# Performance work log

Hardware: AMD Instinct MI355X
Metric: run time of the kernel (lower is better)

The kernel has to match this reference:

```python
import jax, jax.numpy as jnp
import numpy as np

T, H, E, K = 16384, 2880, 128, 4

def setup_inputs() -> dict:
    key = jax.random.key(0)
    k1, k2, k3 = jax.random.split(key, 3)
    return {
        "hidden_states": jax.random.normal(k1, (T, H), dtype=jnp.float32),
        "weight": jax.random.normal(k2, (E, H), dtype=jnp.float32) * 0.02,
        "bias": jax.random.normal(k3, (E,), dtype=jnp.float32) * 0.02,
    }

def reference(hidden_states, weight, bias):
    x = hidden_states.reshape(-1, weight.shape[1])            # [T, H]
    logits = jnp.einsum('th,eh->te', x, weight) + bias        # [T, E]
    top_val, top_idx = jax.lax.top_k(logits, K)               # sorted desc, [T, K]
    top_val = jax.nn.softmax(top_val, axis=-1)
    rows = jnp.arange(logits.shape[0])[:, None]
    scores = jnp.zeros_like(logits).at[rows, top_idx].set(top_val)
    return scores, top_idx
```

## Files before the change

kernel.cpp:

```cpp
#include <hip/hip_runtime.h>
#include <math.h>


#define T_TOK 16384
#define HDIM  2880
#define EEXP  128
#define KTOP  4

#define TM   32
#define NT   256
#define KC   64
#define NCH  (HDIM / KC)
#define XBUF 8192
#define TAU  2.5e-4f

typedef __attribute__((ext_vector_type(8))) short bf16x8;
typedef __attribute__((ext_vector_type(4))) float f32x4;

#define MFMA(a, b, c) __builtin_amdgcn_mfma_f32_16x16x32_bf16((a), (b), (c), 0, 0, 0)

__global__ __launch_bounds__(256) void w_split(
    const float* __restrict__ w, char* __restrict__ wp)
{
    const int gid  = blockIdx.x * 256 + threadIdx.x;
    const int lane = gid & 63;
    const int q    = gid >> 6;
    const int ks   = q & 1;
    const int q2   = q >> 1;
    const int c    = q2 % NCH;
    const int F    = q2 / NCH;
    const int e    = F * 16 + (lane & 15);
    const int k0   = c * 64 + ks * 32 + (lane >> 4) * 8;

    const float* src = w + (size_t)e * HDIM + k0;
    float4 v0 = *(const float4*)(src);
    float4 v1 = *(const float4*)(src + 4);
    float vv[8] = {v0.x, v0.y, v0.z, v0.w, v1.x, v1.y, v1.z, v1.w};
    union { unsigned short s[8]; uint4 u; } H, L;
#pragma unroll
    for (int j = 0; j < 8; ++j) {
        unsigned u = __float_as_uint(vv[j]);
        H.s[j] = (unsigned short)(u >> 16);
        float rr = vv[j] - __uint_as_float(u & 0xffff0000u);
        L.s[j] = (unsigned short)(__float_as_uint(rr) >> 16);
    }
    const int tile = ((F * NCH + c) * 2 + ks) * 2;
    *(uint4*)(wp + (size_t)tile * 1024 + lane * 16)       = H.u;
    *(uint4*)(wp + (size_t)(tile + 1) * 1024 + lane * 16) = L.u;
}

static __device__ __forceinline__ void split_write256(char* base, int off, float4 v) {
    union { float4 v4; unsigned u[4]; } uv; uv.v4 = v;
    unsigned h01 = __builtin_amdgcn_perm(uv.u[1], uv.u[0], 0x07060302u);
    unsigned h23 = __builtin_amdgcn_perm(uv.u[3], uv.u[2], 0x07060302u);
    float r0 = v.x - __uint_as_float(uv.u[0] & 0xffff0000u);
    float r1 = v.y - __uint_as_float(uv.u[1] & 0xffff0000u);
    float r2 = v.z - __uint_as_float(uv.u[2] & 0xffff0000u);
    float r3 = v.w - __uint_as_float(uv.u[3] & 0xffff0000u);
    unsigned l01 = __builtin_amdgcn_perm(__float_as_uint(r1), __float_as_uint(r0), 0x07060302u);
    unsigned l23 = __builtin_amdgcn_perm(__float_as_uint(r3), __float_as_uint(r2), 0x07060302u);
    uint2 hw; hw.x = h01; hw.y = h23;
    uint2 lw; lw.x = l01; lw.y = l23;
    *(uint2*)(base + off)       = hw;
    *(uint2*)(base + off + 128) = lw;
}

__global__ __launch_bounds__(NT, 2) void router_fused(
    const float* __restrict__ x, const char* __restrict__ wp,
    const float* __restrict__ w, const float* __restrict__ bias,
    float* __restrict__ out)
{
    __shared__ char smem[20480];
    const int tid  = threadIdx.x;
    const int tok0 = blockIdx.x * TM;
    const int lane = tid & 63;
    const int wv   = tid >> 6;
    const int r    = lane & 15;
    const int g    = lane >> 4;

    char* xb0 = smem;
    char* xb1 = smem + XBUF;

    int xoff[2];
    const float* xptr[2];
#pragma unroll
    for (int i = 0; i < 2; ++i) {
        int f = tid + i * NT;
        int row = f >> 4, c4 = f & 15;
        xoff[i] = row * 256 + ((((c4 >> 1) ^ (row & 7)) << 4) | ((c4 & 1) << 3));
        xptr[i] = x + (size_t)(tok0 + row) * HDIM + c4 * 4;
    }

    int aoff[2][2];
#pragma unroll
    for (int tf = 0; tf < 2; ++tf) {
        int row = tf * 16 + r;
#pragma unroll
        for (int ks = 0; ks < 2; ++ks)
            aoff[tf][ks] = row * 256 + (((ks * 4 + g) ^ (row & 7)) << 4);
    }

    f32x4 a00 = {0.f, 0.f, 0.f, 0.f}, a01 = a00, a10 = a00, a11 = a00;

#define LOADX(pf, cc) do {                                            \
        pf[0] = *(const float4*)(xptr[0] + (cc) * KC);                \
        pf[1] = *(const float4*)(xptr[1] + (cc) * KC); } while (0)

#define WRITEX(pf, bb) do {                                           \
        split_write256((bb), xoff[0], pf[0]);                         \
        split_write256((bb), xoff[1], pf[1]); } while (0)

#define LOADW(W, cc) do {                                             \
        _Pragma("unroll")                                             \
        for (int F2 = 0; F2 < 2; ++F2)                                \
        _Pragma("unroll")                                             \
        for (int ks_ = 0; ks_ < 2; ++ks_)                             \
        _Pragma("unroll")                                             \
        for (int p_ = 0; p_ < 2; ++p_)                                \
            W[F2*4 + ks_*2 + p_] = *(const bf16x8*)(wp +              \
                (size_t)((((wv*2 + F2) * NCH + (cc)) * 2 + ks_) * 2 + p_) * 1024 \
                + lane * 16); } while (0)

#define MFMA_CHUNK(cb, W) do {                                        \
        _Pragma("unroll")                                             \
        for (int ks_ = 0; ks_ < 2; ++ks_) {                           \
            bf16x8 ah0 = *(const bf16x8*)((cb) + aoff[0][ks_]);       \
            bf16x8 al0 = *(const bf16x8*)((cb) + aoff[0][ks_] + 128); \
            bf16x8 ah1 = *(const bf16x8*)((cb) + aoff[1][ks_]);       \
            bf16x8 al1 = *(const bf16x8*)((cb) + aoff[1][ks_] + 128); \
            bf16x8 bh0 = W[ks_*2],     bl0 = W[ks_*2 + 1];            \
            bf16x8 bh1 = W[4 + ks_*2], bl1 = W[4 + ks_*2 + 1];        \
            a00 = MFMA(ah0, bh0, a00); a01 = MFMA(ah0, bh1, a01);     \
            a10 = MFMA(ah1, bh0, a10); a11 = MFMA(ah1, bh1, a11);     \
            a00 = MFMA(ah0, bl0, a00); a01 = MFMA(ah0, bl1, a01);     \
            a10 = MFMA(ah1, bl0, a10); a11 = MFMA(ah1, bl1, a11);     \
            a00 = MFMA(al0, bh0, a00); a01 = MFMA(al0, bh1, a01);     \
            a10 = MFMA(al1, bh0, a10); a11 = MFMA(al1, bh1, a11);     \
        } } while (0)

    float4 pf[2];
    bf16x8 wA[8], wB[8];

    LOADX(pf, 0);
    LOADW(wA, 0);
    WRITEX(pf, xb0);
    __syncthreads();

    for (int c = 0; c < NCH - 1; c += 2) {
        LOADX(pf, c + 1); LOADW(wB, c + 1);
        MFMA_CHUNK(xb0, wA);
        WRITEX(pf, xb1);
        __syncthreads();
        if (c + 2 < NCH) { LOADX(pf, c + 2); LOADW(wA, c + 2); }
        MFMA_CHUNK(xb1, wB);
        if (c + 2 < NCH) WRITEX(pf, xb0);
        __syncthreads();
    }
    MFMA_CHUNK(xb0, wA);
    __syncthreads();

    float* logitsL = (float*)smem;
    const float bv0 = bias[wv * 32 + r];
    const float bv1 = bias[wv * 32 + 16 + r];
#pragma unroll
    for (int q = 0; q < 4; ++q) {
        int m0 = g * 4 + q, m1 = m0 + 16;
        int e0 = wv * 32 + r, e1 = e0 + 16;
        logitsL[m0 * 130 + e0] = a00[q] + bv0;
        logitsL[m0 * 130 + e1] = a01[q] + bv1;
        logitsL[m1 * 130 + e0] = a10[q] + bv0;
        logitsL[m1 * 130 + e1] = a11[q] + bv1;
    }
    float*  cvf = (float*) (smem + 16640);
    int*    cie = (int*)   (smem + 17664);
    int*    flg = (int*)   (smem + 18688);
    double* svd = (double*)(smem + 18816);
    int*    sid = (int*)   (smem + 19840);
    double* cvd = (double*)(smem + 20352);
    __syncthreads();

    {
        const int t = tid >> 3, s = tid & 7;
        float v[8]; int id[8];
#pragma unroll
        for (int k = 0; k < 8; ++k) { v[k] = -3.4e38f; id[k] = 0x7fffffff; }
        for (int jj = 0; jj < 16; ++jj) {
            float lv = logitsL[t * 130 + s * 16 + jj];
            int   e  = s * 16 + jj;
            bool gt[8];
#pragma unroll
            for (int k = 0; k < 8; ++k)
                gt[k] = (lv > v[k]) || (lv == v[k] && e < id[k]);
#pragma unroll
            for (int k = 7; k >= 1; --k)
                if (gt[k - 1]) { v[k] = v[k - 1]; id[k] = id[k - 1]; }
#pragma unroll
            for (int k = 0; k < 8; ++k) {
                bool put = gt[k] && (k == 0 || !gt[k - 1]);
                if (put) { v[k] = lv; id[k] = e; }
            }
        }
#pragma unroll
        for (int rd = 0; rd < 8; ++rd) {
            float hv = v[0]; int hi = id[0];
#pragma unroll
            for (int off = 1; off < 8; off <<= 1) {
                float ov = __shfl_xor(hv, off);
                int   oi = __shfl_xor(hi, off);
                if (ov > hv || (ov == hv && oi < hi)) { hv = ov; hi = oi; }
            }
            if (s == 0) { cvf[t * 8 + rd] = hv; cie[t * 8 + rd] = hi; }
            bool mine = (v[0] == hv) && (id[0] == hi);
            if (mine) {
#pragma unroll
                for (int k = 0; k < 7; ++k) { v[k] = v[k + 1]; id[k] = id[k + 1]; }
                v[7] = -3.4e38f; id[7] = 0x7fffffff;
            }
        }
    }
    __syncthreads();

    if (tid < TM) {
        float gmin = 3.4e38f;
#pragma unroll
        for (int k = 0; k < 4; ++k)
            gmin = fminf(gmin, cvf[tid * 8 + k] - cvf[tid * 8 + k + 1]);
        flg[tid] = (gmin < TAU);
    }
    if (tid < 128) {
        int t2 = tid >> 2, k = tid & 3;
        svd[t2 * 4 + k] = (double)cvf[t2 * 8 + k];
        sid[t2 * 4 + k] = cie[t2 * 8 + k];
    }
    __syncthreads();

    for (int ts = 0; ts < TM; ++ts) {
        if (!flg[ts]) continue;
#pragma unroll
        for (int h2 = 0; h2 < 2; ++h2) {
            const int cand = wv * 2 + h2;
            const int ce = cie[ts * 8 + cand];
            const float4* xr = (const float4*)(x + (size_t)(tok0 + ts) * HDIM);
            const float4* wr = (const float4*)(w + (size_t)ce * HDIM);
            double q0 = 0.0, q1 = 0.0, q2 = 0.0, q3 = 0.0;
            for (int i2 = 0; i2 < 12; ++i2) {
                int fi = lane + i2 * 64;
                if (fi < HDIM / 4) {
                    float4 xv = xr[fi];
                    float4 wv4 = wr[fi];
                    q0 = fma((double)xv.x, (double)wv4.x, q0);
                    q1 = fma((double)xv.y, (double)wv4.y, q1);
                    q2 = fma((double)xv.z, (double)wv4.z, q2);
                    q3 = fma((double)xv.w, (double)wv4.w, q3);
                }
            }
            double accd = (q0 + q2) + (q1 + q3);
#pragma unroll
            for (int off = 32; off > 0; off >>= 1)
                accd += __shfl_xor(accd, off);
            if (lane == 0) cvd[cand] = accd + (double)bias[ce];
        }
        __syncthreads();
        if (tid < 8) {
            double mv = cvd[tid]; int mi2 = cie[ts * 8 + tid];
            int rk = 0;
#pragma unroll
            for (int j2 = 0; j2 < 8; ++j2) {
                double oj = cvd[j2];
                rk += (oj > mv) || (oj == mv && cie[ts * 8 + j2] < mi2);
            }
            if (rk < 4) { svd[ts * 4 + rk] = mv; sid[ts * 4 + rk] = mi2; }
        }
        __syncthreads();
    }

    float* srow = (float*)smem;
    float4 z4 = make_float4(0.f, 0.f, 0.f, 0.f);
#pragma unroll
    for (int i = 0; i < 4; ++i)
        ((float4*)srow)[tid + i * NT] = z4;
    __syncthreads();

    if (tid < TM) {
        double m  = svd[tid * 4];
        double e0 = exp(svd[tid * 4 + 0] - m), e1 = exp(svd[tid * 4 + 1] - m);
        double e2 = exp(svd[tid * 4 + 2] - m), e3 = exp(svd[tid * 4 + 3] - m);
        double inv = 1.0 / ((e0 + e1) + (e2 + e3));
        float* oidx = out + (size_t)T_TOK * EEXP + (size_t)(tok0 + tid) * KTOP;
        int i0 = sid[tid * 4 + 0], i1 = sid[tid * 4 + 1];
        int i2 = sid[tid * 4 + 2], i3 = sid[tid * 4 + 3];
        oidx[0] = (float)i0; oidx[1] = (float)i1;
        oidx[2] = (float)i2; oidx[3] = (float)i3;
        srow[tid * EEXP + i0] = (float)(e0 * inv);
        srow[tid * EEXP + i1] = (float)(e1 * inv);
        srow[tid * EEXP + i2] = (float)(e2 * inv);
        srow[tid * EEXP + i3] = (float)(e3 * inv);
    }
    __syncthreads();

    float4* orow = (float4*)(out + (size_t)tok0 * EEXP);
#pragma unroll
    for (int i = 0; i < 4; ++i)
        orow[tid + i * NT] = ((float4*)srow)[tid + i * NT];
}

extern "C" void kernel_launch(void* const* d_in, const int* in_sizes, int n_in,
                              void* d_out, int out_size, void* d_ws, size_t ws_size,
                              hipStream_t stream) {
    const float* x    = (const float*)d_in[0];
    const float* w    = (const float*)d_in[1];
    const float* bias = (const float*)d_in[2];
    float* out        = (float*)d_out;
    char*  wp         = (char*)d_ws;

    hipLaunchKernelGGL(w_split, dim3(180), dim3(256), 0, stream, w, wp);
    hipLaunchKernelGGL(router_fused, dim3(T_TOK / TM), dim3(NT), 0, stream,
                       x, wp, w, bias, out);
}
```

Before: 85.09 us.

## Split router GEMM into producer and consumer waves with 4-stage LDS ring

Doubles the block to 512 threads. Four producer waves load x from global memory, split it into bf16 hi/lo and write it into a 4-slot LDS ring. Four consumer waves load the packed weights and run the MFMAs. The two groups hand off through LDS counters with spin-waits (s_sleep) in place of block-wide __syncthreads, so x loading overlaps compute. The launch bound rises to 4 blocks per CU, which may push register pressure to the point of spilling the weight double buffers, and the spin-waits add polling overhead.

```diff
diff --git a/kernel.cpp b/kernel.cpp
--- a/kernel.cpp
+++ b/kernel.cpp
@@ -8,7 +8,7 @@
 #define KTOP  4
 
 #define TM   32
-#define NT   256
+#define NT   512
 #define KC   64
 #define NCH  (HDIM / KC)
 #define XBUF 8192
@@ -65,50 +65,65 @@
     *(uint2*)(base + off + 128) = lw;
 }
 
-__global__ __launch_bounds__(NT, 2) void router_fused(
+__global__ __launch_bounds__(NT, 4) void router_fused(
     const float* __restrict__ x, const char* __restrict__ wp,
     const float* __restrict__ w, const float* __restrict__ bias,
     float* __restrict__ out)
 {
-    __shared__ char smem[20480];
+    __shared__ char smem[4 * XBUF + 64];
     const int tid  = threadIdx.x;
     const int tok0 = blockIdx.x * TM;
     const int lane = tid & 63;
     const int wv   = tid >> 6;
-    const int r    = lane & 15;
-    const int g    = lane >> 4;
-
-    char* xb0 = smem;
-    char* xb1 = smem + XBUF;
-
-    int xoff[2];
-    const float* xptr[2];
-#pragma unroll
-    for (int i = 0; i < 2; ++i) {
-        int f = tid + i * NT;
-        int row = f >> 4, c4 = f & 15;
-        xoff[i] = row * 256 + ((((c4 >> 1) ^ (row & 7)) << 4) | ((c4 & 1) << 3));
-        xptr[i] = x + (size_t)(tok0 + row) * HDIM + c4 * 4;
-    }
-
-    int aoff[2][2];
-#pragma unroll
-    for (int tf = 0; tf < 2; ++tf) {
-        int row = tf * 16 + r;
-#pragma unroll
-        for (int ks = 0; ks < 2; ++ks)
-            aoff[tf][ks] = row * 256 + (((ks * 4 + g) ^ (row & 7)) << 4);
-    }
+
+    volatile unsigned* prod_cnt  = (volatile unsigned*)(smem + 4 * XBUF);
+    volatile unsigned* cons_done = (volatile unsigned*)(smem + 4 * XBUF + 16);
+    if (tid < 4) { ((unsigned*)(smem + 4 * XBUF))[tid] = 0u;
+                   ((unsigned*)(smem + 4 * XBUF + 16))[tid] = 0u; }
+    __syncthreads();
 
     f32x4 a00 = {0.f, 0.f, 0.f, 0.f}, a01 = a00, a10 = a00, a11 = a00;
 
-#define LOADX(pf, cc) do {                                            \
-        pf[0] = *(const float4*)(xptr[0] + (cc) * KC);                \
-        pf[1] = *(const float4*)(xptr[1] + (cc) * KC); } while (0)
-
-#define WRITEX(pf, bb) do {                                           \
-        split_write256((bb), xoff[0], pf[0]);                         \
-        split_write256((bb), xoff[1], pf[1]); } while (0)
+    if (wv < 4) {
+        int xoff[2];
+        const float* xptr[2];
+#pragma unroll
+        for (int i = 0; i < 2; ++i) {
+            int f = tid + i * 256;
+            int row = f >> 4, c4 = f & 15;
+            xoff[i] = row * 256 + ((((c4 >> 1) ^ (row & 7)) << 4) | ((c4 & 1) << 3));
+            xptr[i] = x + (size_t)(tok0 + row) * HDIM + c4 * 4;
+        }
+        float4 pf0 = *(const float4*)(xptr[0]);
+        float4 pf1 = *(const float4*)(xptr[1]);
+        for (int c = 0; c < NCH; ++c) {
+            const int s = c & 3;
+            const unsigned k = (unsigned)(c >> 2);
+            while (cons_done[s] < 4u * k) __builtin_amdgcn_s_sleep(2);
+            asm volatile("" ::: "memory");
+            __builtin_amdgcn_sched_barrier(0);
+            char* bb = smem + s * XBUF;
+            split_write256(bb, xoff[0], pf0);
+            split_write256(bb, xoff[1], pf1);
+            if (c + 1 < NCH) {
+                pf0 = *(const float4*)(xptr[0] + (c + 1) * KC);
+                pf1 = *(const float4*)(xptr[1] + (c + 1) * KC);
+            }
+            asm volatile("s_waitcnt lgkmcnt(0)" ::: "memory");
+            if (lane == 0) atomicAdd((unsigned*)&prod_cnt[s], 1u);
+        }
+    } else {
+        const int cwv = wv - 4;
+        const int r   = lane & 15;
+        const int g   = lane >> 4;
+        int aoff[2][2];
+#pragma unroll
+        for (int tf = 0; tf < 2; ++tf) {
+            int row = tf * 16 + r;
+#pragma unroll
+            for (int ks = 0; ks < 2; ++ks)
+                aoff[tf][ks] = row * 256 + (((ks * 4 + g) ^ (row & 7)) << 4);
+        }
 
 #define LOADW(W, cc) do {                                             \
         _Pragma("unroll")                                             \
@@ -118,7 +133,7 @@
         _Pragma("unroll")                                             \
         for (int p_ = 0; p_ < 2; ++p_)                                \
             W[F2*4 + ks_*2 + p_] = *(const bf16x8*)(wp +              \
-                (size_t)((((wv*2 + F2) * NCH + (cc)) * 2 + ks_) * 2 + p_) * 1024 \
+                (size_t)((((cwv*2 + F2) * NCH + (cc)) * 2 + ks_) * 2 + p_) * 1024 \
                 + lane * 16); } while (0)
 
 #define MFMA_CHUNK(cb, W) do {                                        \
@@ -138,38 +153,46 @@
             a10 = MFMA(al1, bh0, a10); a11 = MFMA(al1, bh1, a11);     \
         } } while (0)
 
-    float4 pf[2];
-    bf16x8 wA[8], wB[8];
-
-    LOADX(pf, 0);
-    LOADW(wA, 0);
-    WRITEX(pf, xb0);
-    __syncthreads();
-
-    for (int c = 0; c < NCH - 1; c += 2) {
-        LOADX(pf, c + 1); LOADW(wB, c + 1);
-        MFMA_CHUNK(xb0, wA);
-        WRITEX(pf, xb1);
-        __syncthreads();
-        if (c + 2 < NCH) { LOADX(pf, c + 2); LOADW(wA, c + 2); }
-        MFMA_CHUNK(xb1, wB);
-        if (c + 2 < NCH) WRITEX(pf, xb0);
-        __syncthreads();
-    }
-    MFMA_CHUNK(xb0, wA);
+#define CONSUME(cc, W) do {                                           \
+        const int s_ = (cc) & 3;                                      \
+        const unsigned k_ = (unsigned)((cc) >> 2);                    \
+        while (prod_cnt[s_] < 4u * (k_ + 1u)) __builtin_amdgcn_s_sleep(2); \
+        asm volatile("" ::: "memory");                                \
+        __builtin_amdgcn_sched_barrier(0);                            \
+        MFMA_CHUNK(smem + s_ * XBUF, W);                              \
+        asm volatile("s_waitcnt lgkmcnt(0)" ::: "memory");            \
+        __builtin_amdgcn_sched_barrier(0);                            \
+        if (lane == 0) atomicAdd((unsigned*)&cons_done[s_], 1u);      \
+    } while (0)
+
+        bf16x8 wA[8], wB[8];
+        LOADW(wA, 0);
+        for (int c = 0; c < 44; c += 2) {
+            LOADW(wB, c + 1);
+            CONSUME(c, wA);
+            LOADW(wA, c + 2);
+            CONSUME(c + 1, wB);
+        }
+        CONSUME(44, wA);
+    }
     __syncthreads();
 
     float* logitsL = (float*)smem;
-    const float bv0 = bias[wv * 32 + r];
-    const float bv1 = bias[wv * 32 + 16 + r];
-#pragma unroll
-    for (int q = 0; q < 4; ++q) {
-        int m0 = g * 4 + q, m1 = m0 + 16;
-        int e0 = wv * 32 + r, e1 = e0 + 16;
-        logitsL[m0 * 130 + e0] = a00[q] + bv0;
-        logitsL[m0 * 130 + e1] = a01[q] + bv1;
-        logitsL[m1 * 130 + e0] = a10[q] + bv0;
-        logitsL[m1 * 130 + e1] = a11[q] + bv1;
+    if (wv >= 4) {
+        const int cwv = wv - 4;
+        const int r   = lane & 15;
+        const int g   = lane >> 4;
+        const float bv0 = bias[cwv * 32 + r];
+        const float bv1 = bias[cwv * 32 + 16 + r];
+#pragma unroll
+        for (int q = 0; q < 4; ++q) {
+            int m0 = g * 4 + q, m1 = m0 + 16;
+            int e0 = cwv * 32 + r, e1 = e0 + 16;
+            logitsL[m0 * 130 + e0] = a00[q] + bv0;
+            logitsL[m0 * 130 + e1] = a01[q] + bv1;
+            logitsL[m1 * 130 + e0] = a10[q] + bv0;
+            logitsL[m1 * 130 + e1] = a11[q] + bv1;
+        }
     }
     float*  cvf = (float*) (smem + 16640);
     int*    cie = (int*)   (smem + 17664);
@@ -179,7 +202,7 @@
     double* cvd = (double*)(smem + 20352);
     __syncthreads();
 
-    {
+    if (tid < 256) {
         const int t = tid >> 3, s = tid & 7;
         float v[8]; int id[8];
 #pragma unroll
@@ -236,10 +259,8 @@
 
     for (int ts = 0; ts < TM; ++ts) {
         if (!flg[ts]) continue;
-#pragma unroll
-        for (int h2 = 0; h2 < 2; ++h2) {
-            const int cand = wv * 2 + h2;
-            const int ce = cie[ts * 8 + cand];
+        {
+            const int ce = cie[ts * 8 + wv];
             const float4* xr = (const float4*)(x + (size_t)(tok0 + ts) * HDIM);
             const float4* wr = (const float4*)(w + (size_t)ce * HDIM);
             double q0 = 0.0, q1 = 0.0, q2 = 0.0, q3 = 0.0;
@@ -258,7 +279,7 @@
 #pragma unroll
             for (int off = 32; off > 0; off >>= 1)
                 accd += __shfl_xor(accd, off);
-            if (lane == 0) cvd[cand] = accd + (double)bias[ce];
+            if (lane == 0) cvd[wv] = accd + (double)bias[ce];
         }
         __syncthreads();
         if (tid < 8) {
@@ -277,7 +298,7 @@
     float* srow = (float*)smem;
     float4 z4 = make_float4(0.f, 0.f, 0.f, 0.f);
 #pragma unroll
-    for (int i = 0; i < 4; ++i)
+    for (int i = 0; i < 2; ++i)
         ((float4*)srow)[tid + i * NT] = z4;
     __syncthreads();
 
@@ -300,7 +321,7 @@
 
     float4* orow = (float4*)(out + (size_t)tok0 * EEXP);
 #pragma unroll
-    for (int i = 0; i < 4; ++i)
+    for (int i = 0; i < 2; ++i)
         orow[tid + i * NT] = ((float4*)srow)[tid + i * NT];
 }
 
```

After: 79.98 us. 1.06x faster.
